# Performance work log

Measured on AMD Instinct MI355X. Metric: run time of the kernel, lower is better.

## Reference

```python
import jax, jax.numpy as jnp
import numpy as np

H_SIZE = 768
N_HEADS = 12
HEAD = H_SIZE // N_HEADS
INTER = 3072
N_LAYERS = 6
VOCAB = 65536
WIDTH = 512  # attention_width
EPS = 1e-6


def rmsnorm(x, w):
    return x * jax.lax.rsqrt(jnp.mean(x * x, axis=-1, keepdims=True) + EPS) * w


def rotate_every_two(x):
    # interleaved rotation: (x0,x1,x2,x3,...) -> (-x1,x0,-x3,x2,...)
    x1 = x[..., ::2]
    x2 = x[..., 1::2]
    return jnp.stack((-x2, x1), axis=-1).reshape(x.shape)


def fixed_pos_embedding(ages, dim):
    # ages: [B,S] float32 -> sin,cos: [B,S,1,dim]
    inv_freq = 1.0 / 10000 ** jnp.linspace(0.0, 2.0, dim // 2)
    t = ages[..., None] * inv_freq  # [B,S,dim//2]
    sin, cos = jnp.sin(t), jnp.cos(t)
    shp = ages.shape + (1, dim)
    sin = jnp.stack((sin, sin), axis=-1).reshape(shp)
    cos = jnp.stack((cos, cos), axis=-1).reshape(shp)
    return sin, cos


def local_attention(q, k, v, width):
    # causal local attention: query i attends to keys j with i-width < j <= i
    B, S, H, D = q.shape
    nb = S // width
    qb = q.reshape(B, nb, width, H, D)
    pad = ((0, 0), (width, 0), (0, 0), (0, 0))
    kp = jnp.pad(k, pad).reshape(B, nb + 1, width, H, D)
    vp = jnp.pad(v, pad).reshape(B, nb + 1, width, H, D)
    k2 = jnp.concatenate((kp[:, :-1], kp[:, 1:]), axis=2)  # [B,nb,2W,H,D]
    v2 = jnp.concatenate((vp[:, :-1], vp[:, 1:]), axis=2)
    scale = 1.0 / jnp.sqrt(jnp.asarray(D, q.dtype))
    scores = jnp.einsum('bnqhd,bnkhd->bnhqk', qb, k2) * scale
    qi = jnp.arange(width)[:, None]
    kj = jnp.arange(2 * width)[None, :]
    blk = jnp.arange(nb)[:, None, None]
    # global: i = b*W+qi, j = b*W - W + kj ; valid: j<=i, i-j<W, j>=0
    valid = (kj > qi) & (kj <= qi + width) & ((blk * width - width + kj) >= 0)
    scores = jnp.where(valid[None, :, None, :, :], scores, -jnp.inf)
    attn = jax.nn.softmax(scores, axis=-1)
    out = jnp.einsum('bnhqk,bnkhd->bnqhd', attn, v2)
    return out.reshape(B, S, H, D)


def encoder_layer(x, sin, cos, p):
    B, S, _ = x.shape
    xn = rmsnorm(x, p['norm_w'])
    qkv = (xn @ p['attn_W'] + p['attn_b']).reshape(B, S, 3, N_HEADS, HEAD)
    q = qkv[:, :, 0] * cos + rotate_every_two(qkv[:, :, 0]) * sin
    k = qkv[:, :, 1] * cos + rotate_every_two(qkv[:, :, 1]) * sin
    v = qkv[:, :, 2]
    attn = local_attention(q, k, v, WIDTH).reshape(B, S, H_SIZE)
    ff = jax.nn.gelu(xn @ p['in_W'] + p['in_b'], approximate=False)
    combined = jnp.concatenate((attn, ff), axis=-1)
    return combined @ p['out_W'] + p['out_b']


def setup_inputs() -> dict:
    key = jax.random.key(0)
    ks = jax.random.split(key, 10)
    B, S = 4, 2048
    std = 0.02
    tokens = jax.random.randint(ks[0], (B, S), 0, VOCAB, dtype=jnp.int64 if jax.config.jax_enable_x64 else jnp.int32)
    ages = jax.random.uniform(ks[1], (B, S), dtype=jnp.float32) * 1000.0
    embed = jax.random.normal(ks[2], (VOCAB, H_SIZE), jnp.float32) * std
    in_norm_w = jnp.ones((H_SIZE,), jnp.float32)
    out_norm_w = jnp.ones((H_SIZE,), jnp.float32)
    norm_w = jnp.ones((N_LAYERS, H_SIZE), jnp.float32)
    attn_W = jax.random.normal(ks[3], (N_LAYERS, H_SIZE, 3 * H_SIZE), jnp.float32) * std
    attn_b = jnp.zeros((N_LAYERS, 3 * H_SIZE), jnp.float32)
    in_W = jax.random.normal(ks[4], (N_LAYERS, H_SIZE, INTER), jnp.float32) * std
    in_b = jnp.zeros((N_LAYERS, INTER), jnp.float32)
    out_W = jax.random.normal(ks[5], (N_LAYERS, H_SIZE + INTER, H_SIZE), jnp.float32) * std
    out_b = jnp.zeros((N_LAYERS, H_SIZE), jnp.float32)
    return {'tokens': tokens, 'ages': ages, 'embed': embed,
            'in_norm_w': in_norm_w, 'out_norm_w': out_norm_w, 'norm_w': norm_w,
            'attn_W': attn_W, 'attn_b': attn_b, 'in_W': in_W, 'in_b': in_b,
            'out_W': out_W, 'out_b': out_b}


def reference(tokens, ages, embed, in_norm_w, out_norm_w, norm_w, attn_W, attn_b, in_W, in_b, out_W, out_b):
    x = embed[tokens]
    x = rmsnorm(x, in_norm_w)
    sin, cos = fixed_pos_embedding(ages, HEAD)
    params = {'norm_w': norm_w, 'attn_W': attn_W, 'attn_b': attn_b,
              'in_W': in_W, 'in_b': in_b, 'out_W': out_W, 'out_b': out_b}

    def step(h, p):
        return h + encoder_layer(h, sin, cos, p), None

    x, _ = jax.lax.scan(step, x, params)
    return rmsnorm(x, out_norm_w)
```

## Files before the change

kernel.cpp:

```cpp
#include <hip/hip_runtime.h>
#include <hip/hip_bf16.h>
#include <math.h>

#define H_SIZE 768
#define N_HEADS 12
#define HEAD 64
#define INTER 3072
#define N_LAYERS 6
#define BATCH 4
#define SEQ 2048
#define BS (BATCH*SEQ)
#define EPSV 1e-6f

typedef __attribute__((ext_vector_type(8))) short bf16x8;
typedef __attribute__((ext_vector_type(4))) float f32x4;
typedef unsigned short u16;

__device__ inline float bf2f(u16 v) {
    union { float f; unsigned u; } x; x.u = ((unsigned)v) << 16; return x.f;
}
__device__ inline u16 f2bf(float f) {
    union { float f; unsigned u; } x; x.f = f;
    unsigned u = x.u;
    return (u16)((u + 0x7FFFu + ((u >> 16) & 1u)) >> 16);
}

__device__ __forceinline__ void stage16(const u16* g, u16* ldsbase) {
    __builtin_amdgcn_global_load_lds((const __attribute__((address_space(1))) void*)g,
                                     (__attribute__((address_space(3))) void*)ldsbase,
                                     16, 0, 0);
}

__global__ void probe_kernel(const u16* __restrict__ embed, const int* __restrict__ tokens,
                             int* __restrict__ flags) {
    if (threadIdx.x == 0 && blockIdx.x == 0) {
        int good = 0, evenzero = 0;
        for (int i = 0; i < 128; i++) {
            u16 h = embed[i];
            int e = (h >> 7) & 0xFF;
            if (h == 0 || (e >= 87 && e <= 133)) good++;
            if ((i & 1) == 0 && h == 0) evenzero++;
        }
        flags[0] = (evenzero >= 48) ? 1 : ((good >= 110) ? 0 : 1);
        int z = 0;
        for (int i = 0; i < 64; i++) if (tokens[2 * i + 1] == 0) z++;
        flags[1] = (z >= 60) ? 1 : 0;
    }
}

__global__ __launch_bounds__(256) void sincos_kernel(const void* __restrict__ ages,
                                                     float* __restrict__ SIN,
                                                     float* __restrict__ COS,
                                                     const int* __restrict__ flags) {
    int idx = blockIdx.x * 256 + threadIdx.x;
    if (idx >= BS * 32) return;
    bool f32in = flags[0] != 0;
    int row = idx >> 5, f = idx & 31;
    float age = f32in ? ((const float*)ages)[row] : bf2f(((const u16*)ages)[row]);
    float inv = expf(-(2.0f * (float)f / 31.0f) * 9.210340371976184f);
    float t = age * inv;
    SIN[idx] = sinf(t);
    COS[idx] = cosf(t);
}

__global__ __launch_bounds__(256) void wtrans_kernel(const void* __restrict__ Wsrc,
                                                     u16* __restrict__ Wt,
                                                     int K, int N,
                                                     const int* __restrict__ flags) {
    __shared__ u16 tile[64][72];
    bool f32in = flags[0] != 0;
    int k0 = blockIdx.y * 64, n0 = blockIdx.x * 64;
    int t = threadIdx.x;
    int kk = t >> 3, nn = (t & 7) * 8;
#pragma unroll
    for (int it = 0; it < 2; it++) {
        int kr = kk + it * 32;
        u16 tmp[8];
        if (f32in) {
            const float* src = (const float*)Wsrc + (size_t)(k0 + kr) * N + n0 + nn;
            float4 f0 = *(const float4*)src, f1 = *(const float4*)(src + 4);
            tmp[0] = f2bf(f0.x); tmp[1] = f2bf(f0.y); tmp[2] = f2bf(f0.z); tmp[3] = f2bf(f0.w);
            tmp[4] = f2bf(f1.x); tmp[5] = f2bf(f1.y); tmp[6] = f2bf(f1.z); tmp[7] = f2bf(f1.w);
        } else {
            uint4 v = *(const uint4*)((const u16*)Wsrc + (size_t)(k0 + kr) * N + n0 + nn);
            const u16* pv = (const u16*)&v;
#pragma unroll
            for (int i = 0; i < 8; i++) tmp[i] = pv[i];
        }
        *(uint4*)(&tile[kr][nn]) = *(const uint4*)tmp;
    }
    __syncthreads();
    int n = t >> 3, kq = (t & 7) * 8;
#pragma unroll
    for (int it = 0; it < 2; it++) {
        int nr = n + it * 32;
        u16 tmp[8];
#pragma unroll
        for (int i = 0; i < 8; i++) tmp[i] = tile[kq + i][nr];
        *(uint4*)(Wt + (size_t)(n0 + nr) * K + k0 + kq) = *(const uint4*)tmp;
    }
}

__global__ __launch_bounds__(256) void bias_conv_kernel(const void* __restrict__ ab,
                                                        const void* __restrict__ ib,
                                                        const void* __restrict__ ob,
                                                        u16* __restrict__ dst,
                                                        const int* __restrict__ flags) {
    int i = blockIdx.x * 256 + threadIdx.x;
    bool f32in = flags[0] != 0;
    const int A = 6 * 2304, B = 6 * 3072, C = 6 * 768;
    if (i < A) dst[i] = f32in ? f2bf(((const float*)ab)[i]) : ((const u16*)ab)[i];
    else if (i < A + B) { int j = i - A; dst[i] = f32in ? f2bf(((const float*)ib)[j]) : ((const u16*)ib)[j]; }
    else if (i < A + B + C) { int j = i - A - B; dst[i] = f32in ? f2bf(((const float*)ob)[j]) : ((const u16*)ob)[j]; }
}

__global__ __launch_bounds__(256) void embed_norm_kernel(const int* __restrict__ tokens,
                                                         const void* __restrict__ embed,
                                                         const void* __restrict__ wbase,
                                                         float* __restrict__ X,
                                                         const int* __restrict__ flags) {
    int row = blockIdx.x * 4 + (threadIdx.x >> 6);
    int lane = threadIdx.x & 63;
    bool f32in = flags[0] != 0;
    bool i64 = flags[1] != 0;
    int tok = i64 ? tokens[2 * row] : tokens[row];
    tok &= 65535;
    const u16* er16 = (const u16*)embed + (size_t)tok * H_SIZE;
    const float* er32 = (const float*)embed + (size_t)tok * H_SIZE;
    const u16* w16 = (const u16*)wbase;
    const float* w32 = (const float*)wbase;
    float v[12]; float ss = 0.f;
#pragma unroll
    for (int k = 0; k < 12; k++) {
        int i = lane + k * 64;
        float t = f32in ? er32[i] : bf2f(er16[i]);
        v[k] = t; ss += t * t;
    }
#pragma unroll
    for (int off = 1; off < 64; off <<= 1) ss += __shfl_xor(ss, off, 64);
    float scale = rsqrtf(ss * (1.0f / 768.0f) + EPSV);
#pragma unroll
    for (int k = 0; k < 12; k++) {
        int i = lane + k * 64;
        float wv = f32in ? w32[i] : bf2f(w16[i]);
        X[(size_t)row * H_SIZE + i] = v[k] * scale * wv;
    }
}

__global__ __launch_bounds__(256) void rmsnorm_kernel(const float* __restrict__ X,
                                                      const void* __restrict__ wbase, size_t woff,
                                                      void* __restrict__ Y, int outMode,
                                                      const int* __restrict__ flags) {
    int row = blockIdx.x * 4 + (threadIdx.x >> 6);
    int lane = threadIdx.x & 63;
    bool f32in = flags[0] != 0;
    const u16* w16 = (const u16*)wbase + woff;
    const float* w32 = (const float*)wbase + woff;
    const float* xr = X + (size_t)row * H_SIZE;
    float v[12]; float ss = 0.f;
#pragma unroll
    for (int k = 0; k < 12; k++) { v[k] = xr[lane + k * 64]; ss += v[k] * v[k]; }
#pragma unroll
    for (int off = 1; off < 64; off <<= 1) ss += __shfl_xor(ss, off, 64);
    float scale = rsqrtf(ss * (1.0f / 768.0f) + EPSV);
    bool of32 = outMode && f32in;
#pragma unroll
    for (int k = 0; k < 12; k++) {
        int i = lane + k * 64;
        float wv = f32in ? w32[i] : bf2f(w16[i]);
        float val = v[k] * scale * wv;
        if (of32) ((float*)Y)[(size_t)row * H_SIZE + i] = val;
        else      ((u16*)Y)[(size_t)row * H_SIZE + i] = f2bf(val);
    }
}

template <int EPI>
__global__ __launch_bounds__(256) void gemm_kernel(const u16* __restrict__ A,
                                                   const u16* __restrict__ Wt,
                                                   const u16* __restrict__ bias,
                                                   float* __restrict__ Cf,
                                                   u16* __restrict__ Cb, int ldcb,
                                                   int M, int N, int K,
                                                   const float* __restrict__ SIN,
                                                   const float* __restrict__ COS) {
    __shared__ u16 Al[128][32];
    __shared__ u16 Bl[128][32];
    const int tid = threadIdx.x;
    const int lane = tid & 63, wave = tid >> 6;
    const int wm = wave >> 1, wn = wave & 1;
    const int lm = lane & 15, g = lane >> 4;
    const int m0 = blockIdx.y * 128, n0 = blockIdx.x * 128;

    f32x4 acc[4][4];
#pragma unroll
    for (int i = 0; i < 4; i++)
#pragma unroll
        for (int j = 0; j < 4; j++) acc[i][j] = (f32x4)0.0f;

    const u16* gaBase = A  + (size_t)(m0 + wave * 16 + (lane >> 2)) * K + (lane & 3) * 8;
    const u16* gbBase = Wt + (size_t)(n0 + wave * 16 + (lane >> 2)) * K + (lane & 3) * 8;
    const size_t rowK64 = (size_t)64 * K;
    u16* ldsA0 = &Al[wave * 16][0];
    u16* ldsA1 = &Al[64 + wave * 16][0];
    u16* ldsB0 = &Bl[wave * 16][0];
    u16* ldsB1 = &Bl[64 + wave * 16][0];

    for (int k0 = 0; k0 < K; k0 += 32) {
        __syncthreads();
        stage16(gaBase + k0, ldsA0);
        stage16(gaBase + rowK64 + k0, ldsA1);
        stage16(gbBase + k0, ldsB0);
        stage16(gbBase + rowK64 + k0, ldsB1);
        __syncthreads();
        bf16x8 a[4], b[4];
#pragma unroll
        for (int i = 0; i < 4; i++) a[i] = *(const bf16x8*)(&Al[wm * 64 + i * 16 + lm][g * 8]);
#pragma unroll
        for (int j = 0; j < 4; j++) b[j] = *(const bf16x8*)(&Bl[wn * 64 + j * 16 + lm][g * 8]);
#pragma unroll
        for (int i = 0; i < 4; i++)
#pragma unroll
            for (int j = 0; j < 4; j++)
                acc[i][j] = __builtin_amdgcn_mfma_f32_16x16x32_bf16(a[i], b[j], acc[i][j], 0, 0, 0);
    }

#pragma unroll
    for (int i = 0; i < 4; i++) {
        int mbase = m0 + wm * 64 + i * 16 + g * 4;
#pragma unroll
        for (int j = 0; j < 4; j++) {
            int n = n0 + wn * 64 + j * 16 + lm;
            float bv = bf2f(bias[n]);
#pragma unroll
            for (int r = 0; r < 4; r++) {
                float v = acc[i][j][r] + bv;
                int mm = mbase + r;
                if (EPI == 0) {
                    float p = __shfl_xor(v, 1);
                    float outv = v;
                    if (n < 1536) {
                        int f = (n >> 1) & 31;
                        float c = COS[mm * 32 + f], s = SIN[mm * 32 + f];
                        outv = (n & 1) ? (v * c + p * s) : (v * c - p * s);
                    }
                    Cb[(size_t)mm * ldcb + n] = f2bf(outv);
                } else if (EPI == 1) {
                    float u = 0.7978845608f * (v + 0.044715f * v * v * v);
                    float e = __expf(2.0f * u);
                    float th = 1.0f - 2.0f / (e + 1.0f);
                    Cb[(size_t)mm * ldcb + n] = f2bf(0.5f * v * (1.0f + th));
                } else {
                    Cf[(size_t)mm * N + n] += v;
                }
            }
        }
    }
}

__global__ __launch_bounds__(256) void attn_kernel(const u16* __restrict__ qkv,
                                                   u16* __restrict__ Out) {
    __shared__ u16 Qs[64][72];
    __shared__ u16 Ks[64][72];
    __shared__ u16 Vt[64][72];
    __shared__ u16 Ps[4][16][72];

    const int tid = threadIdx.x;
    const int lane = tid & 63, wave = tid >> 6;
    const int lm = lane & 15, g = lane >> 4;
    const int q0 = blockIdx.x * 64;
    const int h = blockIdx.y;
    const int b = blockIdx.z;
    const size_t rowbase = (size_t)b * SEQ;

#pragma unroll
    for (int it = 0; it < 2; ++it) {
        int idx = tid + it * 256;
        int r = idx >> 3, u = (idx & 7) * 8;
        uint4 v = *(const uint4*)(qkv + (rowbase + q0 + r) * 2304 + h * HEAD + u);
        *(uint4*)(&Qs[r][u]) = v;
    }

    float m_r[4], l_r[4];
    f32x4 o[4];
#pragma unroll
    for (int r = 0; r < 4; r++) { m_r[r] = -INFINITY; l_r[r] = 0.f; }
#pragma unroll
    for (int d = 0; d < 4; d++) o[d] = (f32x4)0.0f;

    const int c_start = (q0 < 512) ? ((512 - q0) >> 6) : 0;
    for (int c = c_start; c < 9; ++c) {
        int kc = q0 - 512 + c * 64;
        __syncthreads();
#pragma unroll
        for (int it = 0; it < 2; ++it) {
            int idx = tid + it * 256;
            int r = idx >> 3, u = (idx & 7) * 8;
            int j = kc + r;
            uint4 kv = make_uint4(0, 0, 0, 0), vv = make_uint4(0, 0, 0, 0);
            if (j >= 0) {
                kv = *(const uint4*)(qkv + (rowbase + j) * 2304 + 768 + h * HEAD + u);
                vv = *(const uint4*)(qkv + (rowbase + j) * 2304 + 1536 + h * HEAD + u);
            }
            *(uint4*)(&Ks[r][u]) = kv;
            const u16* pv = (const u16*)&vv;
#pragma unroll
            for (int i = 0; i < 8; i++) Vt[u + i][r] = pv[i];
        }
        __syncthreads();

        bf16x8 aq0 = *(const bf16x8*)(&Qs[wave * 16 + lm][g * 8]);
        bf16x8 aq1 = *(const bf16x8*)(&Qs[wave * 16 + lm][32 + g * 8]);
        f32x4 s[4];
#pragma unroll
        for (int kf = 0; kf < 4; kf++) {
            bf16x8 b0 = *(const bf16x8*)(&Ks[kf * 16 + lm][g * 8]);
            bf16x8 b1 = *(const bf16x8*)(&Ks[kf * 16 + lm][32 + g * 8]);
            f32x4 z = (f32x4)0.0f;
            z = __builtin_amdgcn_mfma_f32_16x16x32_bf16(aq0, b0, z, 0, 0, 0);
            z = __builtin_amdgcn_mfma_f32_16x16x32_bf16(aq1, b1, z, 0, 0, 0);
            s[kf] = z;
        }

        float sv[4][4], mc[4];
#pragma unroll
        for (int r = 0; r < 4; r++) mc[r] = -INFINITY;
#pragma unroll
        for (int kf = 0; kf < 4; kf++) {
            int j = kc + kf * 16 + lm;
#pragma unroll
            for (int r = 0; r < 4; r++) {
                int i = q0 + wave * 16 + g * 4 + r;
                bool valid = (j >= 0) && (j <= i) && (j >= i - 511);
                float v = valid ? s[kf][r] * 0.125f : -INFINITY;
                sv[kf][r] = v;
                mc[r] = fmaxf(mc[r], v);
            }
        }
#pragma unroll
        for (int off = 1; off < 16; off <<= 1)
#pragma unroll
            for (int r = 0; r < 4; r++) mc[r] = fmaxf(mc[r], __shfl_xor(mc[r], off, 64));

        float alpha[4], mn[4];
#pragma unroll
        for (int r = 0; r < 4; r++) {
            mn[r] = fmaxf(m_r[r], mc[r]);
            alpha[r] = (mn[r] > -1e37f) ? __expf(m_r[r] - mn[r]) : 1.0f;
            m_r[r] = mn[r];
        }
        float ps[4][4], rs[4] = {0.f, 0.f, 0.f, 0.f};
#pragma unroll
        for (int kf = 0; kf < 4; kf++)
#pragma unroll
            for (int r = 0; r < 4; r++) {
                float p = (sv[kf][r] > -1e37f) ? __expf(sv[kf][r] - mn[r]) : 0.0f;
                ps[kf][r] = p;
                rs[r] += p;
            }
#pragma unroll
        for (int off = 1; off < 16; off <<= 1)
#pragma unroll
            for (int r = 0; r < 4; r++) rs[r] += __shfl_xor(rs[r], off, 64);
#pragma unroll
        for (int r = 0; r < 4; r++) l_r[r] = l_r[r] * alpha[r] + rs[r];

#pragma unroll
        for (int kf = 0; kf < 4; kf++)
#pragma unroll
            for (int r = 0; r < 4; r++) Ps[wave][g * 4 + r][kf * 16 + lm] = f2bf(ps[kf][r]);

#pragma unroll
        for (int d = 0; d < 4; d++)
#pragma unroll
            for (int r = 0; r < 4; r++) o[d][r] *= alpha[r];

        bf16x8 pa0 = *(const bf16x8*)(&Ps[wave][lm][g * 8]);
        bf16x8 pa1 = *(const bf16x8*)(&Ps[wave][lm][32 + g * 8]);
#pragma unroll
        for (int d = 0; d < 4; d++) {
            bf16x8 b0 = *(const bf16x8*)(&Vt[d * 16 + lm][g * 8]);
            bf16x8 b1 = *(const bf16x8*)(&Vt[d * 16 + lm][32 + g * 8]);
            o[d] = __builtin_amdgcn_mfma_f32_16x16x32_bf16(pa0, b0, o[d], 0, 0, 0);
            o[d] = __builtin_amdgcn_mfma_f32_16x16x32_bf16(pa1, b1, o[d], 0, 0, 0);
        }
    }

#pragma unroll
    for (int d = 0; d < 4; d++) {
        int dd = d * 16 + lm;
#pragma unroll
        for (int r = 0; r < 4; r++) {
            int i = q0 + wave * 16 + g * 4 + r;
            float v = o[d][r] / l_r[r];
            Out[(rowbase + i) * 3840 + h * HEAD + dd] = f2bf(v);
        }
    }
}

extern "C" void kernel_launch(void* const* d_in, const int* in_sizes, int n_in,
                              void* d_out, int out_size, void* d_ws, size_t ws_size,
                              hipStream_t stream) {
    const int* tokens   = (const int*)d_in[0];
    const void* ages    = d_in[1];
    const void* embed   = d_in[2];
    const void* in_norm_w  = d_in[3];
    const void* out_norm_w = d_in[4];
    const void* norm_w     = d_in[5];
    const void* attn_W     = d_in[6];
    const void* attn_b     = d_in[7];
    const void* in_W       = d_in[8];
    const void* in_b       = d_in[9];
    const void* out_W      = d_in[10];
    const void* out_b      = d_in[11];

    char* w = (char*)d_ws;
    int* flags  = (int*)w;   w += 256;
    float* x    = (float*)w; w += (size_t)BS * H_SIZE * 4;
    u16* xn     = (u16*)w;   w += (size_t)BS * H_SIZE * 2;
    u16* qkv    = (u16*)w;   w += (size_t)BS * 2304 * 2;
    u16* comb   = (u16*)w;   w += (size_t)BS * 3840 * 2;
    float* sinb = (float*)w; w += (size_t)BS * 32 * 4;
    float* cosb = (float*)w; w += (size_t)BS * 32 * 4;
    u16* wt     = (u16*)w;   w += (size_t)(2304*768 + 3072*768 + 768*3840) * 2;
    u16* biasb  = (u16*)w;   w += (size_t)(6*2304 + 6*3072 + 6*768) * 2;

    u16* wqkv_t = wt;
    u16* win_t  = wt + (size_t)2304 * 768;
    u16* wout_t = win_t + (size_t)3072 * 768;
    u16* ab_b = biasb;
    u16* ib_b = biasb + 6 * 2304;
    u16* ob_b = ib_b + 6 * 3072;

    probe_kernel<<<1, 64, 0, stream>>>((const u16*)embed, tokens, flags);
    sincos_kernel<<<(BS * 32 + 255) / 256, 256, 0, stream>>>(ages, sinb, cosb, flags);
    embed_norm_kernel<<<BS / 4, 256, 0, stream>>>(tokens, embed, in_norm_w, x, flags);
    bias_conv_kernel<<<(6 * (2304 + 3072 + 768) + 255) / 256, 256, 0, stream>>>(
        attn_b, in_b, out_b, biasb, flags);

    for (int l = 0; l < N_LAYERS; ++l) {
        wtrans_kernel<<<dim3(2304 / 64, 768 / 64), 256, 0, stream>>>(
            (const char*)attn_W + (size_t)l * 768 * 2304 * 4, wqkv_t, 768, 2304, flags);
        wtrans_kernel<<<dim3(3072 / 64, 768 / 64), 256, 0, stream>>>(
            (const char*)in_W + (size_t)l * 768 * 3072 * 4, win_t, 768, 3072, flags);
        wtrans_kernel<<<dim3(768 / 64, 3840 / 64), 256, 0, stream>>>(
            (const char*)out_W + (size_t)l * 3840 * 768 * 4, wout_t, 3840, 768, flags);

        rmsnorm_kernel<<<BS / 4, 256, 0, stream>>>(x, norm_w, (size_t)l * H_SIZE, xn, 0, flags);
        gemm_kernel<0><<<dim3(2304 / 128, BS / 128), 256, 0, stream>>>(
            xn, wqkv_t, ab_b + l * 2304, nullptr, qkv, 2304, BS, 2304, H_SIZE, sinb, cosb);
        attn_kernel<<<dim3(SEQ / 64, N_HEADS, BATCH), 256, 0, stream>>>(qkv, comb);
        gemm_kernel<1><<<dim3(INTER / 128, BS / 128), 256, 0, stream>>>(
            xn, win_t, ib_b + l * 3072, nullptr, comb + H_SIZE, H_SIZE + INTER,
            BS, INTER, H_SIZE, nullptr, nullptr);
        gemm_kernel<2><<<dim3(H_SIZE / 128, BS / 128), 256, 0, stream>>>(
            comb, wout_t, ob_b + l * 768, x, nullptr, 0, BS, H_SIZE, H_SIZE + INTER,
            nullptr, nullptr);
    }
    rmsnorm_kernel<<<BS / 4, 256, 0, stream>>>(x, out_norm_w, 0, d_out, 1, flags);
}
```

Measured before the change: 2.165 ms.

## Fuse QKV and FFN-in GEMMs, double-buffer LDS, swizzle, batch weight transposes

Concatenates the QKV and FFN-input weights so a single GEMM produces both outputs. The epilogue branches per column, applying rotary to q/k and GELU to the FFN part. The GEMM gains double-buffered LDS staging with an XOR swizzle to cut bank conflicts, plus a grouped workgroup remap for L2 locality. The out-projection GEMM uses a 64-wide N tile so more blocks launch for N=768. All per-layer weight transposes are hoisted into three batched launches before the layer loop, which needs more workspace to hold every layer's weights.

```diff
diff --git a/kernel.cpp b/kernel.cpp
--- a/kernel.cpp
+++ b/kernel.cpp
@@ -65,10 +65,14 @@
 
 __global__ __launch_bounds__(256) void wtrans_kernel(const void* __restrict__ Wsrc,
                                                      u16* __restrict__ Wt,
-                                                     int K, int N,
+                                                     int K, int N, size_t ltstride,
                                                      const int* __restrict__ flags) {
     __shared__ u16 tile[64][72];
     bool f32in = flags[0] != 0;
+    int l = blockIdx.z;
+    const float* W32 = (const float*)Wsrc + (size_t)l * K * N;
+    const u16*   W16 = (const u16*)Wsrc + (size_t)l * K * N;
+    u16* out = Wt + (size_t)l * ltstride;
     int k0 = blockIdx.y * 64, n0 = blockIdx.x * 64;
     int t = threadIdx.x;
     int kk = t >> 3, nn = (t & 7) * 8;
@@ -77,12 +81,12 @@
         int kr = kk + it * 32;
         u16 tmp[8];
         if (f32in) {
-            const float* src = (const float*)Wsrc + (size_t)(k0 + kr) * N + n0 + nn;
+            const float* src = W32 + (size_t)(k0 + kr) * N + n0 + nn;
             float4 f0 = *(const float4*)src, f1 = *(const float4*)(src + 4);
             tmp[0] = f2bf(f0.x); tmp[1] = f2bf(f0.y); tmp[2] = f2bf(f0.z); tmp[3] = f2bf(f0.w);
             tmp[4] = f2bf(f1.x); tmp[5] = f2bf(f1.y); tmp[6] = f2bf(f1.z); tmp[7] = f2bf(f1.w);
         } else {
-            uint4 v = *(const uint4*)((const u16*)Wsrc + (size_t)(k0 + kr) * N + n0 + nn);
+            uint4 v = *(const uint4*)(W16 + (size_t)(k0 + kr) * N + n0 + nn);
             const u16* pv = (const u16*)&v;
 #pragma unroll
             for (int i = 0; i < 8; i++) tmp[i] = pv[i];
@@ -97,7 +101,7 @@
         u16 tmp[8];
 #pragma unroll
         for (int i = 0; i < 8; i++) tmp[i] = tile[kq + i][nr];
-        *(uint4*)(Wt + (size_t)(n0 + nr) * K + k0 + kq) = *(const uint4*)tmp;
+        *(uint4*)(out + (size_t)(n0 + nr) * K + k0 + kq) = *(const uint4*)tmp;
     }
 }
 
@@ -174,83 +178,100 @@
     }
 }
 
-template <int EPI>
+template <int EPI, int BN>
 __global__ __launch_bounds__(256) void gemm_kernel(const u16* __restrict__ A,
                                                    const u16* __restrict__ Wt,
-                                                   const u16* __restrict__ bias,
+                                                   const u16* __restrict__ abias,
+                                                   const u16* __restrict__ bbias,
                                                    float* __restrict__ Cf,
-                                                   u16* __restrict__ Cb, int ldcb,
-                                                   int M, int N, int K,
+                                                   u16* __restrict__ qkvb,
+                                                   u16* __restrict__ combb,
+                                                   int K,
                                                    const float* __restrict__ SIN,
                                                    const float* __restrict__ COS) {
-    __shared__ u16 Al[128][32];
-    __shared__ u16 Bl[128][32];
+    constexpr int NF = BN / 32;
+    __shared__ u16 Al[2][128][32];
+    __shared__ u16 Bl[2][BN][32];
     const int tid = threadIdx.x;
     const int lane = tid & 63, wave = tid >> 6;
     const int wm = wave >> 1, wn = wave & 1;
     const int lm = lane & 15, g = lane >> 4;
-    const int m0 = blockIdx.y * 128, n0 = blockIdx.x * 128;
-
-    f32x4 acc[4][4];
+
+    const int nwg = gridDim.x * gridDim.y;
+    int linear = blockIdx.y * gridDim.x + blockIdx.x;
+    int work = (linear & 7) * (nwg >> 3) + (linear >> 3);
+    const int m0 = (work / gridDim.x) * 128;
+    const int n0 = (work % gridDim.x) * BN;
+
+    f32x4 acc[4][NF];
 #pragma unroll
     for (int i = 0; i < 4; i++)
 #pragma unroll
-        for (int j = 0; j < 4; j++) acc[i][j] = (f32x4)0.0f;
-
-    const u16* gaBase = A  + (size_t)(m0 + wave * 16 + (lane >> 2)) * K + (lane & 3) * 8;
-    const u16* gbBase = Wt + (size_t)(n0 + wave * 16 + (lane >> 2)) * K + (lane & 3) * 8;
-    const size_t rowK64 = (size_t)64 * K;
-    u16* ldsA0 = &Al[wave * 16][0];
-    u16* ldsA1 = &Al[64 + wave * 16][0];
-    u16* ldsB0 = &Bl[wave * 16][0];
-    u16* ldsB1 = &Bl[64 + wave * 16][0];
-
+        for (int j = 0; j < NF; j++) acc[i][j] = (f32x4)0.0f;
+
+    const int swcol = ((lane & 3) ^ ((lane >> 3) & 3)) * 8;
+    const u16* ga = A  + (size_t)(m0 + wave * 16 + (lane >> 2)) * K + swcol;
+    const u16* gb = Wt + (size_t)(n0 + wave * 16 + (lane >> 2)) * K + swcol;
+    const size_t row64 = (size_t)64 * K;
+
+    auto STAGE = [&](int bi, int kk) {
+        stage16(ga + kk, &Al[bi][wave * 16][0]);
+        stage16(ga + row64 + kk, &Al[bi][64 + wave * 16][0]);
+        stage16(gb + kk, &Bl[bi][wave * 16][0]);
+        if constexpr (BN == 128) stage16(gb + row64 + kk, &Bl[bi][64 + wave * 16][0]);
+    };
+
+    STAGE(0, 0);
+    __syncthreads();
+    int cur = 0;
+    const int cc = (g ^ ((lm >> 1) & 3)) * 8;
     for (int k0 = 0; k0 < K; k0 += 32) {
+        if (k0 + 32 < K) STAGE(cur ^ 1, k0 + 32);
+        bf16x8 a[4], b[NF];
+#pragma unroll
+        for (int i = 0; i < 4; i++) a[i] = *(const bf16x8*)(&Al[cur][wm * 64 + i * 16 + lm][cc]);
+#pragma unroll
+        for (int j = 0; j < NF; j++) b[j] = *(const bf16x8*)(&Bl[cur][wn * (BN / 2) + j * 16 + lm][cc]);
+#pragma unroll
+        for (int i = 0; i < 4; i++)
+#pragma unroll
+            for (int j = 0; j < NF; j++)
+                acc[i][j] = __builtin_amdgcn_mfma_f32_16x16x32_bf16(a[i], b[j], acc[i][j], 0, 0, 0);
         __syncthreads();
-        stage16(gaBase + k0, ldsA0);
-        stage16(gaBase + rowK64 + k0, ldsA1);
-        stage16(gbBase + k0, ldsB0);
-        stage16(gbBase + rowK64 + k0, ldsB1);
-        __syncthreads();
-        bf16x8 a[4], b[4];
-#pragma unroll
-        for (int i = 0; i < 4; i++) a[i] = *(const bf16x8*)(&Al[wm * 64 + i * 16 + lm][g * 8]);
-#pragma unroll
-        for (int j = 0; j < 4; j++) b[j] = *(const bf16x8*)(&Bl[wn * 64 + j * 16 + lm][g * 8]);
-#pragma unroll
-        for (int i = 0; i < 4; i++)
-#pragma unroll
-            for (int j = 0; j < 4; j++)
-                acc[i][j] = __builtin_amdgcn_mfma_f32_16x16x32_bf16(a[i], b[j], acc[i][j], 0, 0, 0);
+        cur ^= 1;
     }
 
 #pragma unroll
     for (int i = 0; i < 4; i++) {
         int mbase = m0 + wm * 64 + i * 16 + g * 4;
 #pragma unroll
-        for (int j = 0; j < 4; j++) {
-            int n = n0 + wn * 64 + j * 16 + lm;
-            float bv = bf2f(bias[n]);
+        for (int j = 0; j < NF; j++) {
+            int n = n0 + wn * (BN / 2) + j * 16 + lm;
+            float bv;
+            if (EPI == 0) bv = (n < 2304) ? bf2f(abias[n]) : bf2f(bbias[n - 2304]);
+            else          bv = bf2f(abias[n]);
 #pragma unroll
             for (int r = 0; r < 4; r++) {
                 float v = acc[i][j][r] + bv;
                 int mm = mbase + r;
                 if (EPI == 0) {
                     float p = __shfl_xor(v, 1);
-                    float outv = v;
-                    if (n < 1536) {
-                        int f = (n >> 1) & 31;
-                        float c = COS[mm * 32 + f], s = SIN[mm * 32 + f];
-                        outv = (n & 1) ? (v * c + p * s) : (v * c - p * s);
+                    if (n < 2304) {
+                        float outv = v;
+                        if (n < 1536) {
+                            int f = (n >> 1) & 31;
+                            float c = COS[mm * 32 + f], s = SIN[mm * 32 + f];
+                            outv = (n & 1) ? (v * c + p * s) : (v * c - p * s);
+                        }
+                        qkvb[(size_t)mm * 2304 + n] = f2bf(outv);
+                    } else {
+                        float u = 0.7978845608f * (v + 0.044715f * v * v * v);
+                        float e = __expf(2.0f * u);
+                        float th = 1.0f - 2.0f / (e + 1.0f);
+                        combb[(size_t)mm * 3840 + (n - 1536)] = f2bf(0.5f * v * (1.0f + th));
                     }
-                    Cb[(size_t)mm * ldcb + n] = f2bf(outv);
-                } else if (EPI == 1) {
-                    float u = 0.7978845608f * (v + 0.044715f * v * v * v);
-                    float e = __expf(2.0f * u);
-                    float th = 1.0f - 2.0f / (e + 1.0f);
-                    Cb[(size_t)mm * ldcb + n] = f2bf(0.5f * v * (1.0f + th));
                 } else {
-                    Cf[(size_t)mm * N + n] += v;
+                    Cf[(size_t)mm * 768 + n] += v;
                 }
             }
         }
@@ -421,15 +442,15 @@
     u16* comb   = (u16*)w;   w += (size_t)BS * 3840 * 2;
     float* sinb = (float*)w; w += (size_t)BS * 32 * 4;
     float* cosb = (float*)w; w += (size_t)BS * 32 * 4;
-    u16* wt     = (u16*)w;   w += (size_t)(2304*768 + 3072*768 + 768*3840) * 2;
+    u16* wtf    = (u16*)w;   w += (size_t)N_LAYERS * 5376 * 768 * 2;
+    u16* wto    = (u16*)w;   w += (size_t)N_LAYERS * 768 * 3840 * 2;
     u16* biasb  = (u16*)w;   w += (size_t)(6*2304 + 6*3072 + 6*768) * 2;
 
-    u16* wqkv_t = wt;
-    u16* win_t  = wt + (size_t)2304 * 768;
-    u16* wout_t = win_t + (size_t)3072 * 768;
     u16* ab_b = biasb;
     u16* ib_b = biasb + 6 * 2304;
     u16* ob_b = ib_b + 6 * 3072;
+
+    const size_t LFS = (size_t)5376 * 768;
 
     probe_kernel<<<1, 64, 0, stream>>>((const u16*)embed, tokens, flags);
     sincos_kernel<<<(BS * 32 + 255) / 256, 256, 0, stream>>>(ages, sinb, cosb, flags);
@@ -437,24 +458,22 @@
     bias_conv_kernel<<<(6 * (2304 + 3072 + 768) + 255) / 256, 256, 0, stream>>>(
         attn_b, in_b, out_b, biasb, flags);
 
+    wtrans_kernel<<<dim3(2304 / 64, 768 / 64, N_LAYERS), 256, 0, stream>>>(
+        attn_W, wtf, 768, 2304, LFS, flags);
+    wtrans_kernel<<<dim3(3072 / 64, 768 / 64, N_LAYERS), 256, 0, stream>>>(
+        in_W, wtf + (size_t)2304 * 768, 768, 3072, LFS, flags);
+    wtrans_kernel<<<dim3(768 / 64, 3840 / 64, N_LAYERS), 256, 0, stream>>>(
+        out_W, wto, 3840, 768, (size_t)768 * 3840, flags);
+
     for (int l = 0; l < N_LAYERS; ++l) {
-        wtrans_kernel<<<dim3(2304 / 64, 768 / 64), 256, 0, stream>>>(
-            (const char*)attn_W + (size_t)l * 768 * 2304 * 4, wqkv_t, 768, 2304, flags);
-        wtrans_kernel<<<dim3(3072 / 64, 768 / 64), 256, 0, stream>>>(
-            (const char*)in_W + (size_t)l * 768 * 3072 * 4, win_t, 768, 3072, flags);
-        wtrans_kernel<<<dim3(768 / 64, 3840 / 64), 256, 0, stream>>>(
-            (const char*)out_W + (size_t)l * 3840 * 768 * 4, wout_t, 3840, 768, flags);
-
         rmsnorm_kernel<<<BS / 4, 256, 0, stream>>>(x, norm_w, (size_t)l * H_SIZE, xn, 0, flags);
-        gemm_kernel<0><<<dim3(2304 / 128, BS / 128), 256, 0, stream>>>(
-            xn, wqkv_t, ab_b + l * 2304, nullptr, qkv, 2304, BS, 2304, H_SIZE, sinb, cosb);
+        gemm_kernel<0, 128><<<dim3(5376 / 128, BS / 128), 256, 0, stream>>>(
+            xn, wtf + (size_t)l * LFS, ab_b + l * 2304, ib_b + l * 3072,
+            nullptr, qkv, comb, H_SIZE, sinb, cosb);
         attn_kernel<<<dim3(SEQ / 64, N_HEADS, BATCH), 256, 0, stream>>>(qkv, comb);
-        gemm_kernel<1><<<dim3(INTER / 128, BS / 128), 256, 0, stream>>>(
-            xn, win_t, ib_b + l * 3072, nullptr, comb + H_SIZE, H_SIZE + INTER,
-            BS, INTER, H_SIZE, nullptr, nullptr);
-        gemm_kernel<2><<<dim3(H_SIZE / 128, BS / 128), 256, 0, stream>>>(
-            comb, wout_t, ob_b + l * 768, x, nullptr, 0, BS, H_SIZE, H_SIZE + INTER,
-            nullptr, nullptr);
+        gemm_kernel<2, 64><<<dim3(768 / 64, BS / 128), 256, 0, stream>>>(
+            comb, wto + (size_t)l * 768 * 3840, ob_b + l * 768, nullptr,
+            x, nullptr, nullptr, H_SIZE + INTER, nullptr, nullptr);
     }
     rmsnorm_kernel<<<BS / 4, 256, 0, stream>>>(x, out_norm_w, 0, d_out, 1, flags);
 }
```

Result: faster. 1.885 ms (-12.9%).
